# Performance work log

Hardware: AMD Instinct MI355X
Metric: run time of the kernel (lower is better)

The kernel has to match this reference:

```python
import jax, jax.numpy as jnp
import numpy as np

SH_DEGREE = 1
D_SH = (SH_DEGREE + 1) ** 2  # 4
SCALE_MIN = 0.5
SCALE_MAX = 15.0
MULTIPLIER = 0.1
EPS = 1e-8


def quat_to_rotmat(q):
    # q: [..., 4] (w, x, y, z), assumed (near-)normalized
    w, x, y, z = q[..., 0], q[..., 1], q[..., 2], q[..., 3]
    return jnp.stack([
        jnp.stack([1 - 2 * (y * y + z * z), 2 * (x * y - w * z), 2 * (x * z + w * y)], -1),
        jnp.stack([2 * (x * y + w * z), 1 - 2 * (x * x + z * z), 2 * (y * z - w * x)], -1),
        jnp.stack([2 * (x * z - w * y), 2 * (y * z + w * x), 1 - 2 * (x * x + y * y)], -1),
    ], -2)


def setup_inputs() -> dict:
    key = jax.random.key(0)
    ks = jax.random.split(key, 6)
    B, N = 8, 131072
    H, W = 256, 512
    # valid SE(3) extrinsics (rotation from random unit quaternion)
    q = jax.random.normal(ks[0], (B, 1, 4), dtype=jnp.float32)
    q = q / jnp.linalg.norm(q, axis=-1, keepdims=True)
    R = quat_to_rotmat(q)
    t = jax.random.normal(ks[1], (B, 1, 3), dtype=jnp.float32)
    ext = jnp.zeros((B, 1, 4, 4), jnp.float32)
    ext = ext.at[..., :3, :3].set(R).at[..., :3, 3].set(t).at[..., 3, 3].set(1.0)
    # normalized pinhole intrinsics
    K = jnp.array([[1.2, 0.0, 0.5], [0.0, 1.2, 0.5], [0.0, 0.0, 1.0]], jnp.float32)
    K = jnp.broadcast_to(K, (B, 1, 3, 3))
    coordinates = jax.random.uniform(ks[2], (B, N, 2), dtype=jnp.float32)
    depths = jax.random.uniform(ks[3], (B, N), dtype=jnp.float32, minval=0.5, maxval=10.0)
    opacities = jax.random.uniform(ks[4], (B, N), dtype=jnp.float32)
    raw_gaussians = jax.random.normal(ks[5], (B, N, 7 + 3 * D_SH), dtype=jnp.float32)
    return {"extrinsics": ext, "intrinsics": K, "coordinates": coordinates,
            "depths": depths, "opacities": opacities, "raw_gaussians": raw_gaussians,
            "h": H, "w": W}


def reference(extrinsics, intrinsics, coordinates, depths, opacities, raw_gaussians, h, w):
    # sh mask: degree-0 untouched, degree d scaled by 0.1 * 0.25**d
    sh_mask = jnp.ones((D_SH,), jnp.float32)
    for d in range(1, SH_DEGREE + 1):
        sh_mask = sh_mask.at[d ** 2:(d + 1) ** 2].set(0.1 * 0.25 ** d)

    scales_raw = raw_gaussians[..., :3]
    rot_raw = raw_gaussians[..., 3:7]
    sh = raw_gaussians[..., 7:]

    scales = SCALE_MIN + (SCALE_MAX - SCALE_MIN) * jax.nn.sigmoid(scales_raw)

    # scale multiplier from inverse of 2x2 top-left of intrinsics
    pixel_size = 1.0 / jnp.array([w, h], jnp.float32)
    a = intrinsics[..., 0, 0]; b = intrinsics[..., 0, 1]
    c = intrinsics[..., 1, 0]; d = intrinsics[..., 1, 1]
    det = a * d - b * c
    inv2 = jnp.stack([jnp.stack([d, -b], -1), jnp.stack([-c, a], -1)], -2) / det[..., None, None]
    multiplier = (MULTIPLIER * jnp.einsum('...ij,j->...i', inv2, pixel_size)).sum(-1)  # [B,1]

    scales = scales * depths[..., None] * multiplier[..., None]  # [B,N,3]

    rotations = rot_raw / (jnp.linalg.norm(rot_raw, axis=-1, keepdims=True) + EPS)  # [B,N,4]

    sh = sh.reshape(*sh.shape[:-1], 3, D_SH) * sh_mask  # [B,N,3,D_SH]

    # covariance = R diag(s^2) R^T, then rotate into world frame
    R = quat_to_rotmat(rotations)  # [B,N,3,3]
    cov = jnp.einsum('...ij,...j,...kj->...ik', R, scales * scales, R)
    c2w = extrinsics[..., :3, :3]  # [B,1,3,3]
    cov = jnp.einsum('...ij,...jk,...lk->...il', c2w, cov, c2w)  # [B,N,3,3]

    # world rays: unproject pixel coords with depth 1, normalize, rotate to world
    coords_h = jnp.concatenate([coordinates, jnp.ones_like(coordinates[..., :1])], -1)  # [B,N,3]
    Kinv = jnp.linalg.inv(intrinsics)  # [B,1,3,3]
    dirs = jnp.einsum('...ij,...j->...i', Kinv, coords_h)
    dirs = dirs / jnp.linalg.norm(dirs, axis=-1, keepdims=True)
    dirs_w = jnp.einsum('...ij,...j->...i', c2w, dirs)  # [B,N,3]
    origins = jnp.broadcast_to(extrinsics[..., :3, 3], dirs_w.shape)
    means = origins + dirs_w * depths[..., None]  # [B,N,3]

    # rotate SH: l=0 identity; l=1 Wigner-D equals c2w in the (y,z,x) permuted basis
    p = jnp.array([1, 2, 0])
    D1 = c2w[..., p, :][..., :, p]  # [B,1,3,3]
    sh0 = sh[..., :1]
    sh1 = jnp.einsum('...ij,...cj->...ci', D1, sh[..., 1:4])
    harmonics = jnp.concatenate([sh0, sh1], -1)  # [B,N,3,D_SH]

    rotations_b = jnp.broadcast_to(rotations, (*scales.shape[:-1], 4))
    return (means, cov, harmonics, opacities, scales, rotations_b)
```

## Files before the change

kernel.cpp:

```cpp
#include <hip/hip_runtime.h>
#include <math.h>

#define SCALE_MIN 0.5f
#define SCALE_MAX 15.0f
#define MULTIPLIER 0.1f
#define EPS 1e-8f

__global__ __launch_bounds__(256) void mono_gaussian_adapter_kernel(
    const float* __restrict__ ext,
    const float* __restrict__ intr,
    const float* __restrict__ coord,
    const float* __restrict__ depth,
    const float* __restrict__ opac,
    const float* __restrict__ rawg,
    const int* __restrict__ hp,
    const int* __restrict__ wp,
    float* __restrict__ out,
    int bpb,
    int BN)
{
    int gid = blockIdx.x * 256 + threadIdx.x;
    if (gid >= BN) return;
    int b = blockIdx.x / bpb;

    float inv_w = 1.0f / (float)wp[0];
    float inv_h = 1.0f / (float)hp[0];

    const float* E = ext + b * 16;
    float c00=E[0],  c01=E[1],  c02=E[2],  t0=E[3];
    float c10=E[4],  c11=E[5],  c12=E[6],  t1=E[7];
    float c20=E[8],  c21=E[9],  c22=E[10], t2=E[11];

    const float* Kb = intr + b * 9;
    float k00=Kb[0],k01=Kb[1],k02=Kb[2];
    float k10=Kb[3],k11=Kb[4],k12=Kb[5];
    float k20=Kb[6],k21=Kb[7],k22=Kb[8];

    float det2 = k00*k11 - k01*k10;
    float mult = MULTIPLIER * ((k11*inv_w - k01*inv_h) + (k00*inv_h - k10*inv_w)) / det2;

    float det3 = k00*(k11*k22 - k12*k21)
               + k01*(k12*k20 - k10*k22)
               + k02*(k10*k21 - k11*k20);
    float id3 = 1.0f / det3;
    float i00 = (k11*k22 - k12*k21)*id3;
    float i01 = (k02*k21 - k01*k22)*id3;
    float i02 = (k01*k12 - k02*k11)*id3;
    float i10 = (k12*k20 - k10*k22)*id3;
    float i11 = (k00*k22 - k02*k20)*id3;
    float i12 = (k02*k10 - k00*k12)*id3;
    float i20 = (k10*k21 - k11*k20)*id3;
    float i21 = (k01*k20 - k00*k21)*id3;
    float i22 = (k00*k11 - k01*k10)*id3;

    float2 uv = ((const float2*)coord)[gid];
    float dep = depth[gid];
    float op  = opac[gid];
    const float* g = rawg + (long long)gid * 19;
    float sr0 = g[0], sr1 = g[1], sr2 = g[2];
    float q0 = g[3], q1 = g[4], q2 = g[5], q3 = g[6];
    float sh00=g[7],  sh01=g[8],  sh02=g[9],  sh03=g[10];
    float sh10=g[11], sh11=g[12], sh12=g[13], sh13=g[14];
    float sh20=g[15], sh21=g[16], sh22=g[17], sh23=g[18];

    float s0 = SCALE_MIN + (SCALE_MAX - SCALE_MIN) / (1.0f + __expf(-sr0));
    float s1 = SCALE_MIN + (SCALE_MAX - SCALE_MIN) / (1.0f + __expf(-sr1));
    float s2 = SCALE_MIN + (SCALE_MAX - SCALE_MIN) / (1.0f + __expf(-sr2));
    float dm = dep * mult;
    s0 *= dm; s1 *= dm; s2 *= dm;

    float qn = sqrtf(q0*q0 + q1*q1 + q2*q2 + q3*q3) + EPS;
    float qi = 1.0f / qn;
    float qw = q0*qi, qx = q1*qi, qy = q2*qi, qz = q3*qi;

    float r00 = 1.0f - 2.0f*(qy*qy + qz*qz);
    float r01 = 2.0f*(qx*qy - qw*qz);
    float r02 = 2.0f*(qx*qz + qw*qy);
    float r10 = 2.0f*(qx*qy + qw*qz);
    float r11 = 1.0f - 2.0f*(qx*qx + qz*qz);
    float r12 = 2.0f*(qy*qz - qw*qx);
    float r20 = 2.0f*(qx*qz - qw*qy);
    float r21 = 2.0f*(qy*qz + qw*qx);
    float r22 = 1.0f - 2.0f*(qx*qx + qy*qy);

    float v0 = s0*s0, v1 = s1*s1, v2 = s2*s2;
    float p00 = r00*r00*v0 + r01*r01*v1 + r02*r02*v2;
    float p01 = r00*r10*v0 + r01*r11*v1 + r02*r12*v2;
    float p02 = r00*r20*v0 + r01*r21*v1 + r02*r22*v2;
    float p11 = r10*r10*v0 + r11*r11*v1 + r12*r12*v2;
    float p12 = r10*r20*v0 + r11*r21*v1 + r12*r22*v2;
    float p22 = r20*r20*v0 + r21*r21*v1 + r22*r22*v2;

    float m00 = c00*p00 + c01*p01 + c02*p02;
    float m01 = c00*p01 + c01*p11 + c02*p12;
    float m02 = c00*p02 + c01*p12 + c02*p22;
    float m10 = c10*p00 + c11*p01 + c12*p02;
    float m11 = c10*p01 + c11*p11 + c12*p12;
    float m12 = c10*p02 + c11*p12 + c12*p22;
    float m20 = c20*p00 + c21*p01 + c22*p02;
    float m21 = c20*p01 + c21*p11 + c22*p12;
    float m22 = c20*p02 + c21*p12 + c22*p22;

    float q00 = m00*c00 + m01*c01 + m02*c02;
    float q01 = m00*c10 + m01*c11 + m02*c12;
    float q02 = m00*c20 + m01*c21 + m02*c22;
    float q11 = m10*c10 + m11*c11 + m12*c12;
    float q12 = m10*c20 + m11*c21 + m12*c22;
    float q22 = m20*c20 + m21*c21 + m22*c22;

    float d0 = i00*uv.x + i01*uv.y + i02;
    float d1 = i10*uv.x + i11*uv.y + i12;
    float d2 = i20*uv.x + i21*uv.y + i22;
    float rn = rsqrtf(d0*d0 + d1*d1 + d2*d2);
    d0 *= rn; d1 *= rn; d2 *= rn;
    float w0 = c00*d0 + c01*d1 + c02*d2;
    float w1 = c10*d0 + c11*d1 + c12*d2;
    float w2 = c20*d0 + c21*d1 + c22*d2;
    float me0 = t0 + w0*dep;
    float me1 = t1 + w1*dep;
    float me2 = t2 + w2*dep;

    float D00=c11, D01=c12, D02=c10;
    float D10=c21, D11=c22, D12=c20;
    float D20=c01, D21=c02, D22=c00;
    const float msk = 0.1f * 0.25f;
    float a1 = msk*sh01, a2 = msk*sh02, a3 = msk*sh03;
    float b1 = msk*sh11, b2 = msk*sh12, b3 = msk*sh13;
    float e1 = msk*sh21, e2 = msk*sh22, e3 = msk*sh23;
    float4 h0 = make_float4(sh00, D00*a1 + D01*a2 + D02*a3,
                                  D10*a1 + D11*a2 + D12*a3,
                                  D20*a1 + D21*a2 + D22*a3);
    float4 h1 = make_float4(sh10, D00*b1 + D01*b2 + D02*b3,
                                  D10*b1 + D11*b2 + D12*b3,
                                  D20*b1 + D21*b2 + D22*b3);
    float4 h2 = make_float4(sh20, D00*e1 + D01*e2 + D02*e3,
                                  D10*e1 + D11*e2 + D12*e3,
                                  D20*e1 + D21*e2 + D22*e3);

    float* om = out + gid*3;
    om[0] = me0; om[1] = me1; om[2] = me2;

    float* oc = out + 3*BN + gid*9;
    oc[0]=q00; oc[1]=q01; oc[2]=q02;
    oc[3]=q01; oc[4]=q11; oc[5]=q12;
    oc[6]=q02; oc[7]=q12; oc[8]=q22;

    float4* oh = (float4*)(out + 12*BN + (long long)gid*12);
    oh[0] = h0; oh[1] = h1; oh[2] = h2;

    out[24*BN + gid] = op;

    float* os = out + 25*BN + gid*3;
    os[0] = s0; os[1] = s1; os[2] = s2;

    ((float4*)(out + 28*BN))[gid] = make_float4(qw, qx, qy, qz);
}

extern "C" void kernel_launch(void* const* d_in, const int* in_sizes, int n_in,
                              void* d_out, int out_size, void* d_ws, size_t ws_size,
                              hipStream_t stream) {
    const float* ext   = (const float*)d_in[0];
    const float* intr  = (const float*)d_in[1];
    const float* coord = (const float*)d_in[2];
    const float* depth = (const float*)d_in[3];
    const float* opac  = (const float*)d_in[4];
    const float* rawg  = (const float*)d_in[5];
    const int*   hp    = (const int*)d_in[6];
    const int*   wp    = (const int*)d_in[7];

    int BN = in_sizes[3];
    int B  = in_sizes[0] / 16;
    int N  = BN / B;
    int blocks = (BN + 255) / 256;
    int bpb = (N + 255) / 256;

    mono_gaussian_adapter_kernel<<<blocks, 256, 0, stream>>>(
        ext, intr, coord, depth, opac, rawg, hp, wp,
        (float*)d_out, bpb, BN);
}
```

Measured before the change: 233.3 us.

## Stage strided input loads and AoS output stores through LDS for coalescing

The kernel now loads each block's 19-float-per-gaussian raw parameters into shared memory with coalesced float4 loads, and each thread reads its own record from LDS. The mean, covariance, harmonics and scale outputs are written to LDS first and then copied to global memory as coalesced float4 stores. This targets the uncoalesced stride-19, stride-9 and stride-3 global accesses of a memory-bound kernel, at the cost of about 27KB of LDS per block and extra barriers. The bounds check is removed and the grid now assumes BN and N are multiples of 256.

```diff
diff --git a/kernel.cpp b/kernel.cpp
--- a/kernel.cpp
+++ b/kernel.cpp
@@ -5,6 +5,15 @@
 #define SCALE_MAX 15.0f
 #define MULTIPLIER 0.1f
 #define EPS 1e-8f
+
+
+#define G 256
+
+#define L_MEAN  0
+#define L_COV   768
+#define L_HARM  3072
+#define L_SCALE 6144
+#define L_TOT   6912
 
 __global__ __launch_bounds__(256) void mono_gaussian_adapter_kernel(
     const float* __restrict__ ext,
@@ -19,9 +28,22 @@
     int bpb,
     int BN)
 {
-    int gid = blockIdx.x * 256 + threadIdx.x;
-    if (gid >= BN) return;
-    int b = blockIdx.x / bpb;
+    __shared__ float lds[L_TOT];
+
+    const int tid = threadIdx.x;
+    const int blk = blockIdx.x;
+    const int gid = blk * G + tid;
+    const int b = blk / bpb;
+
+    {
+        const float4* gin = (const float4*)(rawg + (long long)blk * (G * 19));
+        float4* l4 = (float4*)lds;
+        #pragma unroll
+        for (int i = 0; i < 5; ++i) {
+            int idx = tid + i * 256;
+            if (idx < (G * 19 / 4)) l4[idx] = gin[idx];
+        }
+    }
 
     float inv_w = 1.0f / (float)wp[0];
     float inv_h = 1.0f / (float)hp[0];
@@ -56,12 +78,17 @@
     float2 uv = ((const float2*)coord)[gid];
     float dep = depth[gid];
     float op  = opac[gid];
-    const float* g = rawg + (long long)gid * 19;
+
+    __syncthreads();
+
+    const float* g = lds + tid * 19;
     float sr0 = g[0], sr1 = g[1], sr2 = g[2];
     float q0 = g[3], q1 = g[4], q2 = g[5], q3 = g[6];
     float sh00=g[7],  sh01=g[8],  sh02=g[9],  sh03=g[10];
     float sh10=g[11], sh11=g[12], sh12=g[13], sh13=g[14];
     float sh20=g[15], sh21=g[16], sh22=g[17], sh23=g[18];
+
+    __syncthreads();
 
     float s0 = SCALE_MIN + (SCALE_MAX - SCALE_MIN) / (1.0f + __expf(-sr0));
     float s1 = SCALE_MIN + (SCALE_MAX - SCALE_MIN) / (1.0f + __expf(-sr1));
@@ -137,23 +164,45 @@
                                   D10*e1 + D11*e2 + D12*e3,
                                   D20*e1 + D21*e2 + D22*e3);
 
-    float* om = out + gid*3;
-    om[0] = me0; om[1] = me1; om[2] = me2;
-
-    float* oc = out + 3*BN + gid*9;
-    oc[0]=q00; oc[1]=q01; oc[2]=q02;
-    oc[3]=q01; oc[4]=q11; oc[5]=q12;
-    oc[6]=q02; oc[7]=q12; oc[8]=q22;
-
-    float4* oh = (float4*)(out + 12*BN + (long long)gid*12);
-    oh[0] = h0; oh[1] = h1; oh[2] = h2;
-
     out[24*BN + gid] = op;
-
-    float* os = out + 25*BN + gid*3;
-    os[0] = s0; os[1] = s1; os[2] = s2;
-
     ((float4*)(out + 28*BN))[gid] = make_float4(qw, qx, qy, qz);
+
+    {
+        float* lm = lds + L_MEAN + tid * 3;
+        lm[0] = me0; lm[1] = me1; lm[2] = me2;
+
+        float* lc = lds + L_COV + tid * 9;
+        lc[0]=q00; lc[1]=q01; lc[2]=q02;
+        lc[3]=q01; lc[4]=q11; lc[5]=q12;
+        lc[6]=q02; lc[7]=q12; lc[8]=q22;
+
+        float4* lh = (float4*)(lds + L_HARM + tid * 12);
+        lh[0] = h0; lh[1] = h1; lh[2] = h2;
+
+        float* ls = lds + L_SCALE + tid * 3;
+        ls[0] = s0; ls[1] = s1; ls[2] = s2;
+    }
+    __syncthreads();
+
+    {
+        const float4* l4 = (const float4*)lds;
+        float4* gm = (float4*)(out + (long long)blk * (3 * G));
+        if (tid < 192) gm[tid] = l4[(L_MEAN / 4) + tid];
+        float4* gs = (float4*)(out + 25LL * BN + (long long)blk * (3 * G));
+        if (tid < 192) gs[tid] = l4[(L_SCALE / 4) + tid];
+        float4* gc = (float4*)(out + 3LL * BN + (long long)blk * (9 * G));
+        #pragma unroll
+        for (int i = 0; i < 3; ++i) {
+            int idx = tid + i * 256;
+            if (idx < 576) gc[idx] = l4[(L_COV / 4) + idx];
+        }
+        float4* gh = (float4*)(out + 12LL * BN + (long long)blk * (12 * G));
+        #pragma unroll
+        for (int i = 0; i < 3; ++i) {
+            int idx = tid + i * 256;
+            gh[idx] = l4[(L_HARM / 4) + idx];
+        }
+    }
 }
 
 extern "C" void kernel_launch(void* const* d_in, const int* in_sizes, int n_in,
@@ -171,8 +220,8 @@
     int BN = in_sizes[3];
     int B  = in_sizes[0] / 16;
     int N  = BN / B;
-    int blocks = (BN + 255) / 256;
-    int bpb = (N + 255) / 256;
+    int blocks = BN / 256;
+    int bpb = N / 256;
 
     mono_gaussian_adapter_kernel<<<blocks, 256, 0, stream>>>(
         ext, intr, coord, depth, opac, rawg, hp, wp,
```

Result: faster. 226.7 us (-2.8%).
